# Performance work log

Hardware: AMD Instinct MI355X
Metric: run time of the kernel (lower is better)

The kernel has to match this reference:

```python
import jax, jax.numpy as jnp
import numpy as np

N1, F_IN, E1 = 50000, 128, 1000000   # data1: 10 graphs x 5000 nodes
B, NPG = 10, 5000
N2, E2 = 199, 4000                    # data2: fixed by fc1 in-dim 9950 = 50*199
K = 50
LN_EPS = 1e-5


def setup_inputs() -> dict:
    key = jax.random.key(0)
    ks = jax.random.split(key, 24)
    s = lambda k, shape: (jax.random.normal(k, shape, jnp.float32) * 0.05)
    inp = {}
    inp["x1"] = jax.random.normal(ks[0], (N1, F_IN), jnp.float32)
    inp["edge_index1"] = jax.random.randint(ks[1], (2, E1), 0, N1, jnp.int32)
    inp["batch1"] = jnp.repeat(jnp.arange(B, dtype=jnp.int32), NPG)  # equal-size graphs
    inp["x2"] = jax.random.normal(ks[2], (N2, F_IN), jnp.float32)
    inp["edge_index2"] = jax.random.randint(ks[3], (2, E2), 0, N2, jnp.int32)
    # GNN params (shared Siamese weights). PyG SAGEConv: lin_l (aggr, has bias), lin_r (root, no bias)
    inp["w1l"] = s(ks[4], (128, F_IN)); inp["b1l"] = jnp.zeros((128,), jnp.float32)
    inp["w1r"] = s(ks[5], (128, F_IN))
    inp["w2l"] = s(ks[6], (64, 128));   inp["b2l"] = jnp.zeros((64,), jnp.float32)
    inp["w2r"] = s(ks[7], (64, 128))
    # MLP head
    inp["fc1_w"] = s(ks[8], (128, K * N2)); inp["fc1_b"] = jnp.zeros((128,), jnp.float32)
    inp["ln1_g"] = jnp.ones((128,), jnp.float32); inp["ln1_b"] = jnp.zeros((128,), jnp.float32)
    inp["fc2_w"] = s(ks[9], (64, 128)); inp["fc2_b"] = jnp.zeros((64,), jnp.float32)
    inp["ln2_g"] = jnp.ones((64,), jnp.float32); inp["ln2_b"] = jnp.zeros((64,), jnp.float32)
    inp["fc3_w"] = s(ks[10], (1, 64)); inp["fc3_b"] = jnp.zeros((1,), jnp.float32)
    return inp


def _sage(x, edge_index, wl, bl, wr, n_nodes):
    # mean aggregation of source features at target nodes, then two linears
    src, dst = edge_index[0], edge_index[1]
    msg_sum = jax.ops.segment_sum(x[src], dst, num_segments=n_nodes)
    cnt = jax.ops.segment_sum(jnp.ones((edge_index.shape[1], 1), x.dtype), dst,
                              num_segments=n_nodes)
    mean = msg_sum / jnp.maximum(cnt, 1.0)
    return mean @ wl.T + bl + x @ wr.T


def _gnn(x, ei, w1l, b1l, w1r, w2l, b2l, w2r):
    n = x.shape[0]
    h = jax.nn.relu(_sage(x, ei, w1l, b1l, w1r, n))
    return jax.nn.relu(_sage(h, ei, w2l, b2l, w2r, n))


def _layernorm(x, g, b):
    mu = jnp.mean(x, -1, keepdims=True)
    var = jnp.mean((x - mu) ** 2, -1, keepdims=True)
    return (x - mu) * jax.lax.rsqrt(var + LN_EPS) * g + b


def reference(x1, edge_index1, batch1, x2, edge_index2,
              w1l, b1l, w1r, w2l, b2l, w2r,
              fc1_w, fc1_b, ln1_g, ln1_b, fc2_w, fc2_b, ln2_g, ln2_b, fc3_w, fc3_b):
    out1 = _gnn(x1, edge_index1, w1l, b1l, w1r, w2l, b2l, w2r)   # [N1, 64]
    out2 = _gnn(x2, edge_index2, w1l, b1l, w1r, w2l, b2l, w2r)   # [N2, 64]
    # cdist p=2
    a2 = jnp.sum(out1 * out1, -1, keepdims=True)                 # [N1,1]
    b2 = jnp.sum(out2 * out2, -1)                                # [N2]
    d2 = a2 + b2[None, :] - 2.0 * (out1 @ out2.T)
    dist = jnp.sqrt(jnp.maximum(d2, 0.0))                        # [N1, N2]
    # SortAggregation(k=50): per-graph sort rows by last column (desc), take top k.
    # batch1 groups equal-size graphs contiguously -> reshape is exact dense batching.
    xb = dist.reshape(B, NPG, N2)
    order = jnp.argsort(-xb[:, :, -1], axis=1)[:, :K]            # [B, K]
    topk = jnp.take_along_axis(xb, order[:, :, None], axis=1)    # [B, K, N2]
    out = topk.reshape(B, K * N2)
    out = jax.nn.relu(_layernorm(out @ fc1_w.T + fc1_b, ln1_g, ln1_b))
    out = jax.nn.relu(_layernorm(out @ fc2_w.T + fc2_b, ln2_g, ln2_b))
    out = jax.nn.sigmoid(out @ fc3_w.T + fc3_b)                  # [B, 1]
    return out
```

## Files before the change

### kernel.cpp

```cpp
#include <hip/hip_runtime.h>
#include <math.h>

#define N1 50000
#define F_IN 128
#define E1 1000000
#define Bg 10
#define NPG 5000
#define N2 199
#define E2 4000
#define KSEL 50
#define LN_EPS 1e-5f
#define CHUNKS 16
#define CHSZ 313
#define EBT 4096
#define NB 196
#define BCAP 6144

typedef unsigned long long ull;

__global__ void k_bucket(const int* __restrict__ ei1, int* __restrict__ bcnt,
                         unsigned int* __restrict__ bed,
                         const int* __restrict__ ei2, int* __restrict__ rp2,
                         int* __restrict__ srcs2) {
  int t = threadIdx.x;
  int blk = blockIdx.x;
  const int nEdgeBlocks = (E1 + EBT - 1) / EBT;
  if (blk == nEdgeBlocks) {
    __shared__ int cnt2[N2];
    __shared__ int cur2[N2];
    const int* src = ei2;
    const int* dst = ei2 + E2;
    for (int i = t; i < N2; i += 256) cnt2[i] = 0;
    __syncthreads();
    for (int e = t; e < E2; e += 256) atomicAdd(&cnt2[dst[e]], 1);
    __syncthreads();
    if (t == 0) {
      int run = 0;
      rp2[0] = 0;
      for (int i = 0; i < N2; i++) {
        cur2[i] = run;
        run += cnt2[i];
        rp2[i + 1] = run;
      }
    }
    __syncthreads();
    for (int e = t; e < E2; e += 256) {
      int d = dst[e];
      int pos = atomicAdd(&cur2[d], 1);
      srcs2[pos] = src[e];
    }
    return;
  }
  __shared__ int hcnt[NB];
  const int* src = ei1;
  const int* dst = ei1 + E1;
  int e0 = blk * EBT;
  int e1 = min(e0 + EBT, E1);
  if (t < NB) hcnt[t] = 0;
  __syncthreads();
  for (int e = e0 + t; e < e1; e += 256) atomicAdd(&hcnt[dst[e] >> 8], 1);
  __syncthreads();
  if (t < NB) hcnt[t] = atomicAdd(&bcnt[t], hcnt[t]);
  __syncthreads();
  for (int e = e0 + t; e < e1; e += 256) {
    int d = dst[e];
    int s = src[e];
    int b = d >> 8;
    int pos = atomicAdd(&hcnt[b], 1);
    if (pos < BCAP)
      bed[(size_t)b * BCAP + pos] = ((unsigned int)(d & 255) << 16) | (unsigned int)s;
  }
}

__global__ __launch_bounds__(1024) void k_csr_bucket(
    const int* __restrict__ bcnt, const unsigned int* __restrict__ bed,
    int* __restrict__ rp, int* __restrict__ srcs) {
  __shared__ int cnt[256];
  __shared__ int cur[256];
  __shared__ int wsums[4];
  __shared__ int s_bbase;
  int b = blockIdx.x, t = threadIdx.x;
  int lane = t & 63, w = t >> 6;
  int total = min(bcnt[b], BCAP);
  if (t < 256) cnt[t] = 0;
  if (w == 0) {
    int vb = 0;
    for (int i = lane; i < b; i += 64) vb += min(bcnt[i], BCAP);
    for (int off = 32; off; off >>= 1) vb += __shfl_xor(vb, off);
    if (lane == 0) s_bbase = vb;
  }
  __syncthreads();
  const unsigned int* list = bed + (size_t)b * BCAP;
  for (int e = t; e < total; e += 1024) atomicAdd(&cnt[list[e] >> 16], 1);
  __syncthreads();
  int incl = 0, v = 0;
  if (t < 256) {
    v = cnt[t];
    int x = v;
#pragma unroll
    for (int off = 1; off < 64; off <<= 1) {
      int y = __shfl_up(x, off);
      if (lane >= off) x += y;
    }
    if (lane == 63) wsums[w] = x;
    incl = x;
  }
  __syncthreads();
  if (t < 256) {
    int pre = 0;
    for (int i = 0; i < w; i++) pre += wsums[i];
    incl += pre;
    int bbase = s_bbase;
    int node = b * 256 + t;
    if (node < N1) rp[node + 1] = bbase + incl;
    cur[t] = bbase + incl - v;
    if (b == 0 && t == 0) rp[0] = 0;
  }
  __syncthreads();
  for (int e = t; e < total; e += 1024) {
    unsigned int pe = list[e];
    int pos = atomicAdd(&cur[pe >> 16], 1);
    srcs[pos] = (int)(pe & 0xFFFFu);
  }
}

__global__ void k_aggr128(const float* __restrict__ xA, const int* __restrict__ rpA,
                          const int* __restrict__ srcsA, float* __restrict__ meanA, int nA,
                          const float* __restrict__ xB, const int* __restrict__ rpB,
                          const int* __restrict__ srcsB, float* __restrict__ meanB, int nB,
                          int blocksA) {
  int blk = blockIdx.x;
  const float* x;
  const int* rp;
  const int* srcs;
  float* mean;
  int n, nb0;
  if (blk < blocksA) { x = xA; rp = rpA; srcs = srcsA; mean = meanA; n = nA; nb0 = blk * 4; }
  else { x = xB; rp = rpB; srcs = srcsB; mean = meanB; n = nB; nb0 = (blk - blocksA) * 4; }
  int lane = threadIdx.x & 63;
  int node = nb0 + (threadIdx.x >> 6);
  if (node >= n) return;
  int s = rp[node], e = rp[node + 1];
  int deg = e - s;
  int half = lane >> 5;
  int sub = lane & 31;
  const float4* xp = (const float4*)x;
  float4 acc = make_float4(0.f, 0.f, 0.f, 0.f);
  int sv = 0;
  if (s + lane < e) sv = srcs[s + lane];
  int lim = deg < 64 ? deg : 64;
  int i = 0;
  for (; i + 8 <= lim; i += 8) {
    int s0 = __shfl(sv, i + half);
    int s1 = __shfl(sv, i + 2 + half);
    int s2 = __shfl(sv, i + 4 + half);
    int s3 = __shfl(sv, i + 6 + half);
    float4 v0 = xp[(size_t)s0 * 32 + sub];
    float4 v1 = xp[(size_t)s1 * 32 + sub];
    float4 v2 = xp[(size_t)s2 * 32 + sub];
    float4 v3 = xp[(size_t)s3 * 32 + sub];
    acc.x += (v0.x + v1.x) + (v2.x + v3.x);
    acc.y += (v0.y + v1.y) + (v2.y + v3.y);
    acc.z += (v0.z + v1.z) + (v2.z + v3.z);
    acc.w += (v0.w + v1.w) + (v2.w + v3.w);
  }
  for (; i + 2 <= lim; i += 2) {
    int s0 = __shfl(sv, i + half);
    float4 v = xp[(size_t)s0 * 32 + sub];
    acc.x += v.x; acc.y += v.y; acc.z += v.z; acc.w += v.w;
  }
  if (i < lim) {
    int s0 = __shfl(sv, i);
    if (half == 0) {
      float4 v = xp[(size_t)s0 * 32 + sub];
      acc.x += v.x; acc.y += v.y; acc.z += v.z; acc.w += v.w;
    }
    i = lim;
  }
  if (deg > 64) {
    int ii = s + 64;
    for (; ii + 8 <= e; ii += 8) {
      int s0 = srcs[ii + half];
      int s1 = srcs[ii + 2 + half];
      int s2 = srcs[ii + 4 + half];
      int s3 = srcs[ii + 6 + half];
      float4 v0 = xp[(size_t)s0 * 32 + sub];
      float4 v1 = xp[(size_t)s1 * 32 + sub];
      float4 v2 = xp[(size_t)s2 * 32 + sub];
      float4 v3 = xp[(size_t)s3 * 32 + sub];
      acc.x += (v0.x + v1.x) + (v2.x + v3.x);
      acc.y += (v0.y + v1.y) + (v2.y + v3.y);
      acc.z += (v0.z + v1.z) + (v2.z + v3.z);
      acc.w += (v0.w + v1.w) + (v2.w + v3.w);
    }
    for (; ii + 2 <= e; ii += 2) {
      int s0 = srcs[ii + half];
      float4 v = xp[(size_t)s0 * 32 + sub];
      acc.x += v.x; acc.y += v.y; acc.z += v.z; acc.w += v.w;
    }
    if (ii < e && half == 0) {
      float4 v = xp[(size_t)srcs[ii] * 32 + sub];
      acc.x += v.x; acc.y += v.y; acc.z += v.z; acc.w += v.w;
    }
  }
  acc.x += __shfl_xor(acc.x, 32);
  acc.y += __shfl_xor(acc.y, 32);
  acc.z += __shfl_xor(acc.z, 32);
  acc.w += __shfl_xor(acc.w, 32);
  if (half == 0) {
    float c = (float)(deg > 0 ? deg : 1);
    float inv = 1.f / c;
    float4 o = make_float4(acc.x * inv, acc.y * inv, acc.z * inv, acc.w * inv);
    ((float4*)mean)[(size_t)node * 32 + sub] = o;
  }
}

__global__ void k_aggr_fused64(const float* __restrict__ zA, const int* __restrict__ rpA,
                               const int* __restrict__ srcsA, float* __restrict__ outA, int nA,
                               const float* __restrict__ zB, const int* __restrict__ rpB,
                               const int* __restrict__ srcsB, float* __restrict__ outB, int nB,
                               const float* __restrict__ bias, int blocksA) {
  int blk = blockIdx.x;
  const float* zlr;
  const int* rp;
  const int* srcs;
  float* out;
  int n, nb0;
  if (blk < blocksA) { zlr = zA; rp = rpA; srcs = srcsA; out = outA; n = nA; nb0 = blk * 4; }
  else { zlr = zB; rp = rpB; srcs = srcsB; out = outB; n = nB; nb0 = (blk - blocksA) * 4; }
  int lane = threadIdx.x & 63;
  int node = nb0 + (threadIdx.x >> 6);
  if (node >= n) return;
  int s = rp[node], e = rp[node + 1];
  int deg = e - s;
  int q = lane >> 4;
  int sub = lane & 15;
  const float4* zp = (const float4*)zlr;
  float4 acc = make_float4(0.f, 0.f, 0.f, 0.f);
  int sv = 0;
  if (s + lane < e) sv = srcs[s + lane];
  int lim = deg < 64 ? deg : 64;
  int i = 0;
  for (; i + 8 <= lim; i += 8) {
    int s0 = __shfl(sv, i + q);
    int s1 = __shfl(sv, i + 4 + q);
    float4 v0 = zp[(size_t)s0 * 32 + sub];
    float4 v1 = zp[(size_t)s1 * 32 + sub];
    acc.x += v0.x + v1.x;
    acc.y += v0.y + v1.y;
    acc.z += v0.z + v1.z;
    acc.w += v0.w + v1.w;
  }
  for (; i + 4 <= lim; i += 4) {
    int s0 = __shfl(sv, i + q);
    float4 v = zp[(size_t)s0 * 32 + sub];
    acc.x += v.x; acc.y += v.y; acc.z += v.z; acc.w += v.w;
  }
  {
    int rem = lim - i;
    int s0 = __shfl(sv, i + q);
    if (q < rem) {
      float4 v = zp[(size_t)s0 * 32 + sub];
      acc.x += v.x; acc.y += v.y; acc.z += v.z; acc.w += v.w;
    }
    i = lim;
  }
  if (deg > 64) {
    int ii = s + 64;
    for (; ii + 8 <= e; ii += 8) {
      int s0 = srcs[ii + q];
      int s1 = srcs[ii + 4 + q];
      float4 v0 = zp[(size_t)s0 * 32 + sub];
      float4 v1 = zp[(size_t)s1 * 32 + sub];
      acc.x += v0.x + v1.x;
      acc.y += v0.y + v1.y;
      acc.z += v0.z + v1.z;
      acc.w += v0.w + v1.w;
    }
    for (; ii + 4 <= e; ii += 4) {
      int s0 = srcs[ii + q];
      float4 v = zp[(size_t)s0 * 32 + sub];
      acc.x += v.x; acc.y += v.y; acc.z += v.z; acc.w += v.w;
    }
    int rem = e - ii;
    if (q < rem) {
      int s0 = srcs[ii + q];
      float4 v = zp[(size_t)s0 * 32 + sub];
      acc.x += v.x; acc.y += v.y; acc.z += v.z; acc.w += v.w;
    }
  }
  acc.x += __shfl_xor(acc.x, 16);
  acc.y += __shfl_xor(acc.y, 16);
  acc.z += __shfl_xor(acc.z, 16);
  acc.w += __shfl_xor(acc.w, 16);
  acc.x += __shfl_xor(acc.x, 32);
  acc.y += __shfl_xor(acc.y, 32);
  acc.z += __shfl_xor(acc.z, 32);
  acc.w += __shfl_xor(acc.w, 32);
  if (q == 0) {
    float c = (float)(deg > 0 ? deg : 1);
    float inv = 1.f / c;
    float4 mb = ((const float4*)bias)[sub];
    float4 rt = zp[(size_t)node * 32 + 16 + sub];
    float v0 = acc.x * inv + mb.x + rt.x;
    float v1 = acc.y * inv + mb.y + rt.y;
    float v2 = acc.z * inv + mb.z + rt.z;
    float v3 = acc.w * inv + mb.w + rt.w;
    float4 o;
    o.x = v0 > 0.f ? v0 : 0.f;
    o.y = v1 > 0.f ? v1 : 0.f;
    o.z = v2 > 0.f ? v2 : 0.f;
    o.w = v3 > 0.f ? v3 : 0.f;
    ((float4*)out)[(size_t)node * 16 + sub] = o;
  }
}

__global__ __launch_bounds__(256) void k_sage_lin(
    const float* __restrict__ xinA, const float* __restrict__ meanA,
    float* __restrict__ zA, int nA,
    const float* __restrict__ xinB, const float* __restrict__ meanB,
    float* __restrict__ zB, int nB,
    const float* __restrict__ w1l, const float* __restrict__ b1l,
    const float* __restrict__ w1r,
    const float* __restrict__ w2l, const float* __restrict__ w2r, int blocksA) {
  constexpr int TM = 128, TK = 32;
  constexpr int SA = TM + 4;
  constexpr int SW = 128 + 4;
  __shared__ float s_a[TK][SA];
  __shared__ float s_w[TK][SW];
  int blk = blockIdx.x;
  const float* xin;
  const float* mean;
  float* zlr;
  int n, m0;
  if (blk < blocksA) { xin = xinA; mean = meanA; zlr = zA; n = nA; m0 = blk * TM; }
  else { xin = xinB; mean = meanB; zlr = zB; n = nB; m0 = (blk - blocksA) * TM; }
  int t = threadIdx.x;
  int tx = t & 15, ty = t >> 4;
  int sub = t >> 3;
  int kv = (t & 7) << 2;

  float acc[8][8];
#pragma unroll
  for (int i = 0; i < 8; i++)
#pragma unroll
    for (int j = 0; j < 8; j++) acc[i][j] = 0.f;

  for (int ph = 0; ph < 2; ph++) {
    const float* A = ph ? xin : mean;
    const float* W = ph ? w1r : w1l;
    for (int k0 = 0; k0 < 128; k0 += TK) {
      __syncthreads();
#pragma unroll
      for (int p = 0; p < 4; p++) {
        int node = m0 + p * 32 + sub;
        float4 v = make_float4(0.f, 0.f, 0.f, 0.f);
        if (node < n) v = *(const float4*)&A[(size_t)node * 128 + k0 + kv];
        int col = p * 32 + sub;
        s_a[kv + 0][col] = v.x;
        s_a[kv + 1][col] = v.y;
        s_a[kv + 2][col] = v.z;
        s_a[kv + 3][col] = v.w;
      }
#pragma unroll
      for (int p = 0; p < 4; p++) {
        int j = p * 32 + sub;
        float4 v = *(const float4*)&W[(size_t)j * 128 + k0 + kv];
        s_w[kv + 0][j] = v.x;
        s_w[kv + 1][j] = v.y;
        s_w[kv + 2][j] = v.z;
        s_w[kv + 3][j] = v.w;
      }
      __syncthreads();
#pragma unroll 8
      for (int kk = 0; kk < TK; kk++) {
        float4 a0 = *(const float4*)&s_a[kk][ty * 8];
        float4 a1 = *(const float4*)&s_a[kk][ty * 8 + 4];
        float av[8] = {a0.x, a0.y, a0.z, a0.w, a1.x, a1.y, a1.z, a1.w};
        float4 w0 = *(const float4*)&s_w[kk][tx * 8];
        float4 w1 = *(const float4*)&s_w[kk][tx * 8 + 4];
        float wv[8] = {w0.x, w0.y, w0.z, w0.w, w1.x, w1.y, w1.z, w1.w};
#pragma unroll
        for (int i = 0; i < 8; i++)
#pragma unroll
          for (int j = 0; j < 8; j++) acc[i][j] = fmaf(av[i], wv[j], acc[i][j]);
      }
    }
  }
  float h[8][8];
  {
    float bj[8];
#pragma unroll
    for (int j = 0; j < 8; j++) bj[j] = b1l[tx * 8 + j];
#pragma unroll
    for (int i = 0; i < 8; i++)
#pragma unroll
      for (int j = 0; j < 8; j++) {
        float v = acc[i][j] + bj[j];
        h[i][j] = v > 0.f ? v : 0.f;
        acc[i][j] = 0.f;
      }
  }
  for (int k0 = 0; k0 < 128; k0 += TK) {
    __syncthreads();
    int txk = tx - (k0 >> 3);
    if (txk >= 0 && txk < 4) {
#pragma unroll
      for (int i = 0; i < 8; i++)
#pragma unroll
        for (int j = 0; j < 8; j++) s_a[txk * 8 + j][ty * 8 + i] = h[i][j];
    }
#pragma unroll
    for (int p = 0; p < 4; p++) {
      int j = p * 32 + sub;
      const float* W = (j < 64) ? &w2l[(size_t)j * 128] : &w2r[(size_t)(j - 64) * 128];
      float4 v = *(const float4*)&W[k0 + kv];
      s_w[kv + 0][j] = v.x;
      s_w[kv + 1][j] = v.y;
      s_w[kv + 2][j] = v.z;
      s_w[kv + 3][j] = v.w;
    }
    __syncthreads();
#pragma unroll 8
    for (int kk = 0; kk < TK; kk++) {
      float4 a0 = *(const float4*)&s_a[kk][ty * 8];
      float4 a1 = *(const float4*)&s_a[kk][ty * 8 + 4];
      float av[8] = {a0.x, a0.y, a0.z, a0.w, a1.x, a1.y, a1.z, a1.w};
      float4 w0 = *(const float4*)&s_w[kk][tx * 8];
      float4 w1 = *(const float4*)&s_w[kk][tx * 8 + 4];
      float wv[8] = {w0.x, w0.y, w0.z, w0.w, w1.x, w1.y, w1.z, w1.w};
#pragma unroll
      for (int i = 0; i < 8; i++)
#pragma unroll
        for (int j = 0; j < 8; j++) acc[i][j] = fmaf(av[i], wv[j], acc[i][j]);
    }
  }
#pragma unroll
  for (int i = 0; i < 8; i++) {
    int node = m0 + ty * 8 + i;
    if (node < n) {
#pragma unroll
      for (int q = 0; q < 8; q += 4) {
        float4 o = make_float4(acc[i][q + 0], acc[i][q + 1], acc[i][q + 2], acc[i][q + 3]);
        *(float4*)&zlr[(size_t)node * 128 + tx * 8 + q] = o;
      }
    }
  }
}

__global__ void k_score_topk_local(const float* __restrict__ out1,
                                   const float* __restrict__ out2,
                                   ull* __restrict__ cand) {
  __shared__ ull s[512];
  __shared__ float brow[64];
  int blk = blockIdx.x;
  int b = blk >> 4, c = blk & 15;
  int t = threadIdx.x;
  if (t < 64) brow[t] = out2[198 * 64 + t];
  __syncthreads();
  const float4* b4 = (const float4*)brow;
  float b2 = 0.f;
#pragma unroll
  for (int q = 0; q < 16; q++) {
    float4 w = b4[q];
    b2 = fmaf(w.x, w.x, fmaf(w.y, w.y, fmaf(w.z, w.z, fmaf(w.w, w.w, b2))));
  }
#pragma unroll
  for (int p = 0; p < 2; p++) {
    int i = p * 256 + t;
    ull key = 0ULL;
    int gidx = c * CHSZ + i;
    if (i < CHSZ && gidx < NPG) {
      const float4* ap = (const float4*)&out1[((size_t)b * NPG + gidx) * 64];
      float dot = 0.f, a2 = 0.f;
#pragma unroll
      for (int q = 0; q < 16; q++) {
        float4 a = ap[q];
        float4 w = b4[q];
        dot = fmaf(a.x, w.x, fmaf(a.y, w.y, fmaf(a.z, w.z, fmaf(a.w, w.w, dot))));
        a2 = fmaf(a.x, a.x, fmaf(a.y, a.y, fmaf(a.z, a.z, fmaf(a.w, a.w, a2))));
      }
      float d2 = a2 + b2 - 2.f * dot;
      float sc = sqrtf(fmaxf(d2, 0.f));
      key = ((ull)__float_as_uint(sc) << 32) | (unsigned int)(~gidx);
    }
    s[i] = key;
  }
  __syncthreads();
  for (int k = 2; k <= 512; k <<= 1) {
    for (int j = k >> 1; j > 0; j >>= 1) {
#pragma unroll
      for (int p = 0; p < 2; p++) {
        int i = p * 256 + t;
        int l = i ^ j;
        if (l > i) {
          bool up = ((i & k) != 0);
          ull a = s[i], bb = s[l];
          if ((a > bb) == up) { s[i] = bb; s[l] = a; }
        }
      }
      __syncthreads();
    }
  }
  if (t < KSEL) cand[(b * CHUNKS + c) * KSEL + t] = s[t];
}

__global__ void k_topk_merge(const ull* __restrict__ cand, int* __restrict__ sel) {
  __shared__ ull s[1024];
  int b = blockIdx.x, t = threadIdx.x;
#pragma unroll
  for (int p = 0; p < 4; p++) {
    int i = p * 256 + t;
    s[i] = (i < CHUNKS * KSEL) ? cand[b * CHUNKS * KSEL + i] : 0ULL;
  }
  __syncthreads();
  for (int k = 2; k <= 1024; k <<= 1) {
    for (int j = k >> 1; j > 0; j >>= 1) {
#pragma unroll
      for (int p = 0; p < 4; p++) {
        int i = p * 256 + t;
        int l = i ^ j;
        if (l > i) {
          bool up = ((i & k) != 0);
          ull a = s[i], bb = s[l];
          if ((a > bb) == up) { s[i] = bb; s[l] = a; }
        }
      }
      __syncthreads();
    }
  }
  if (t < KSEL) {
    int gidx = (int)(~((unsigned int)s[t]));
    sel[b * KSEL + t] = b * NPG + gidx;
  }
}

__global__ void k_dist_rows(const float* __restrict__ out1, const float* __restrict__ out2,
                            const int* __restrict__ sel, float* __restrict__ D) {
  __shared__ float arow[64];
  int i = blockIdx.x;
  int t = threadIdx.x;
  int node = sel[i];
  if (t < 64) arow[t] = out1[(size_t)node * 64 + t];
  __syncthreads();
  float a2 = 0.f;
#pragma unroll
  for (int f = 0; f < 64; f++) a2 = fmaf(arow[f], arow[f], a2);
  for (int nn = t; nn < N2; nn += 256) {
    float dot = 0.f, b2 = 0.f;
#pragma unroll 8
    for (int f = 0; f < 64; f++) {
      float bv = out2[nn * 64 + f];
      dot = fmaf(arow[f], bv, dot);
      b2 = fmaf(bv, bv, b2);
    }
    float d2 = a2 + b2 - 2.f * dot;
    D[i * N2 + nn] = sqrtf(fmaxf(d2, 0.f));
  }
}

__global__ void k_fc1_dot(const float* __restrict__ D, const float* __restrict__ w,
                          float* __restrict__ h1pre) {
  constexpr int M = KSEL * N2;
  constexpr int M2 = M / 2;
  int j = blockIdx.x;
  int t = threadIdx.x;
  const float2* wp = (const float2*)(w + (size_t)j * M);
  float acc[Bg];
#pragma unroll
  for (int b = 0; b < Bg; b++) acc[b] = 0.f;
  for (int m = t; m < M2; m += 256) {
    float2 wv = wp[m];
#pragma unroll
    for (int b = 0; b < Bg; b++) {
      float2 dv = ((const float2*)(D + (size_t)b * M))[m];
      acc[b] = fmaf(dv.x, wv.x, fmaf(dv.y, wv.y, acc[b]));
    }
  }
  __shared__ float ws_[4][Bg];
  int lane = t & 63, wv_ = t >> 6;
#pragma unroll
  for (int b = 0; b < Bg; b++) {
    float v = acc[b];
    for (int off = 32; off; off >>= 1) v += __shfl_xor(v, off);
    if (lane == 0) ws_[wv_][b] = v;
  }
  __syncthreads();
  if (t < Bg) h1pre[t * 128 + j] = ws_[0][t] + ws_[1][t] + ws_[2][t] + ws_[3][t];
}

__global__ void k_fc123(const float* __restrict__ h1pre, const float* __restrict__ fc1b,
                        const float* __restrict__ g1, const float* __restrict__ be1,
                        const float* __restrict__ w2, const float* __restrict__ b2v,
                        const float* __restrict__ g2, const float* __restrict__ be2,
                        const float* __restrict__ w3, const float* __restrict__ b3,
                        float* __restrict__ out) {
  __shared__ float wsum[2];
  __shared__ float sh[128];
  int b = blockIdx.x, t = threadIdx.x;
  float acc = h1pre[b * 128 + t] + fc1b[t];
  int lane = t & 63, wv_ = t >> 6;
  float ssum = acc;
  for (int off = 32; off; off >>= 1) ssum += __shfl_xor(ssum, off);
  if (lane == 0) wsum[wv_] = ssum;
  __syncthreads();
  float mu = (wsum[0] + wsum[1]) / 128.f;
  __syncthreads();
  float d = acc - mu;
  float vv = d * d;
  for (int off = 32; off; off >>= 1) vv += __shfl_xor(vv, off);
  if (lane == 0) wsum[wv_] = vv;
  __syncthreads();
  float var = (wsum[0] + wsum[1]) / 128.f;
  float r = rsqrtf(var + LN_EPS);
  float h = d * r * g1[t] + be1[t];
  sh[t] = h > 0.f ? h : 0.f;
  __syncthreads();
  if (t < 64) {
    float a2 = b2v[t];
#pragma unroll 8
    for (int k = 0; k < 128; k++) a2 = fmaf(sh[k], w2[t * 128 + k], a2);
    float s2 = a2;
    for (int off = 32; off; off >>= 1) s2 += __shfl_xor(s2, off);
    float mu2 = s2 * (1.f / 64.f);
    float d2 = a2 - mu2;
    float vv2 = d2 * d2;
    for (int off = 32; off; off >>= 1) vv2 += __shfl_xor(vv2, off);
    float r2 = rsqrtf(vv2 * (1.f / 64.f) + LN_EPS);
    float h2 = d2 * r2 * g2[t] + be2[t];
    h2 = h2 > 0.f ? h2 : 0.f;
    float pp = h2 * w3[t];
    for (int off = 32; off; off >>= 1) pp += __shfl_xor(pp, off);
    if (t == 0) out[b] = 1.f / (1.f + expf(-(pp + b3[0])));
  }
}

extern "C" void kernel_launch(void* const* d_in, const int* in_sizes, int n_in,
                              void* d_out, int out_size, void* d_ws, size_t ws_size,
                              hipStream_t stream) {
  const float* x1 = (const float*)d_in[0];
  const int* ei1 = (const int*)d_in[1];
  const float* x2 = (const float*)d_in[3];
  const int* ei2 = (const int*)d_in[4];
  const float* w1l = (const float*)d_in[5];
  const float* b1l = (const float*)d_in[6];
  const float* w1r = (const float*)d_in[7];
  const float* w2l = (const float*)d_in[8];
  const float* b2l = (const float*)d_in[9];
  const float* w2r = (const float*)d_in[10];
  const float* fc1w = (const float*)d_in[11];
  const float* fc1b = (const float*)d_in[12];
  const float* ln1g = (const float*)d_in[13];
  const float* ln1b = (const float*)d_in[14];
  const float* fc2w = (const float*)d_in[15];
  const float* fc2b = (const float*)d_in[16];
  const float* ln2g = (const float*)d_in[17];
  const float* ln2b = (const float*)d_in[18];
  const float* fc3w = (const float*)d_in[19];
  const float* fc3b = (const float*)d_in[20];
  float* out = (float*)d_out;

  char* p = (char*)d_ws;
  auto alloc = [&](size_t bytes) {
    char* r = p;
    p += (bytes + 255) & ~(size_t)255;
    return r;
  };
  int* rp1 = (int*)alloc((N1 + 1) * 4);
  int* bcnt = (int*)alloc(NB * 4);
  unsigned int* bed = (unsigned int*)alloc((size_t)NB * BCAP * 4);
  int* srcs1 = (int*)alloc((size_t)E1 * 4);
  int* rp2 = (int*)alloc((N2 + 1) * 4);
  int* srcs2 = (int*)alloc(E2 * 4);
  float* bufMean = (float*)alloc((size_t)N1 * 128 * 4);
  float* bufZ = (float*)alloc((size_t)N1 * 128 * 4);
  float* out1b = (float*)alloc((size_t)N1 * 64 * 4);
  float* mean2 = (float*)alloc((size_t)N2 * 128 * 4);
  float* z2g = (float*)alloc((size_t)N2 * 128 * 4);
  float* out2b = (float*)alloc((size_t)N2 * 64 * 4);
  int* sel = (int*)alloc(Bg * KSEL * 4);
  ull* cand = (ull*)alloc((size_t)Bg * CHUNKS * KSEL * 8);
  float* Dm = (float*)alloc((size_t)Bg * KSEL * N2 * 4);
  float* h1pre = (float*)alloc(Bg * 128 * 4);

  const int nEdgeBlocks = (E1 + EBT - 1) / EBT;
  const int aggrBlocksA = (N1 + 3) / 4;
  const int aggrBlocksB = (N2 + 3) / 4;
  const int gemmBlocksA = (N1 + 127) / 128;
  const int gemmBlocksB = (N2 + 127) / 128;

  hipMemsetAsync(bcnt, 0, NB * 4, stream);
  k_bucket<<<nEdgeBlocks + 1, 256, 0, stream>>>(ei1, bcnt, bed, ei2, rp2, srcs2);
  k_csr_bucket<<<NB, 1024, 0, stream>>>(bcnt, bed, rp1, srcs1);
  k_aggr128<<<aggrBlocksA + aggrBlocksB, 256, 0, stream>>>(
      x1, rp1, srcs1, bufMean, N1, x2, rp2, srcs2, mean2, N2, aggrBlocksA);
  k_sage_lin<<<gemmBlocksA + gemmBlocksB, 256, 0, stream>>>(
      x1, bufMean, bufZ, N1, x2, mean2, z2g, N2, w1l, b1l, w1r, w2l, w2r, gemmBlocksA);
  k_aggr_fused64<<<aggrBlocksA + aggrBlocksB, 256, 0, stream>>>(
      bufZ, rp1, srcs1, out1b, N1, z2g, rp2, srcs2, out2b, N2, b2l, aggrBlocksA);
  k_score_topk_local<<<Bg * CHUNKS, 256, 0, stream>>>(out1b, out2b, cand);
  k_topk_merge<<<Bg, 256, 0, stream>>>(cand, sel);
  k_dist_rows<<<Bg * KSEL, 256, 0, stream>>>(out1b, out2b, sel, Dm);
  k_fc1_dot<<<128, 256, 0, stream>>>(Dm, fc1w, h1pre);
  k_fc123<<<Bg, 128, 0, stream>>>(h1pre, fc1b, ln1g, ln1b, fc2w, fc2b, ln2g, ln2b,
                                  fc3w, fc3b, out);
}
```

Measured before the change: 386.1 us.

## Register-prefetch next K-chunk in fused SAGE linear and pad weight smem layout

Merges the three GEMM phases of the fused SAGE linear kernel into one 12-chunk loop that loads the next chunk's activation and weight tiles into registers while the current chunk is computed. This aims to hide global-memory latency behind the FMA loop. It also remaps the shared weight tile to a 12-float stride per thread group to reduce LDS bank conflicts on the float4 reads. The register prefetch buffers plus h and acc raise register pressure, which may lower occupancy.

```diff
diff --git a/kernel.cpp b/kernel.cpp
--- a/kernel.cpp
+++ b/kernel.cpp
@@ -325,9 +325,9 @@
     const float* __restrict__ w2l, const float* __restrict__ w2r, int blocksA) {
   constexpr int TM = 128, TK = 32;
   constexpr int SA = TM + 4;
-  constexpr int SW = 128 + 4;
+  constexpr int SWS = 196;
   __shared__ float s_a[TK][SA];
-  __shared__ float s_w[TK][SW];
+  __shared__ float s_w[TK][SWS];
   int blk = blockIdx.x;
   const float* xin;
   const float* mean;
@@ -339,86 +339,73 @@
   int tx = t & 15, ty = t >> 4;
   int sub = t >> 3;
   int kv = (t & 7) << 2;
+  int wg = sub >> 3, wo = sub & 7;
 
   float acc[8][8];
 #pragma unroll
   for (int i = 0; i < 8; i++)
 #pragma unroll
     for (int j = 0; j < 8; j++) acc[i][j] = 0.f;
-
-  for (int ph = 0; ph < 2; ph++) {
-    const float* A = ph ? xin : mean;
-    const float* W = ph ? w1r : w1l;
-    for (int k0 = 0; k0 < 128; k0 += TK) {
-      __syncthreads();
+  float h[8][8];
+  float4 ra[4], rw[4];
+
+#pragma unroll
+  for (int p = 0; p < 4; p++) {
+    int node = m0 + p * 32 + sub;
+    ra[p] = make_float4(0.f, 0.f, 0.f, 0.f);
+    if (node < n) ra[p] = *(const float4*)&mean[(size_t)node * 128 + kv];
+    rw[p] = *(const float4*)&w1l[(size_t)(p * 32 + sub) * 128 + kv];
+  }
+
+  for (int c = 0; c < 12; c++) {
+    __syncthreads();
+    if (c < 8) {
 #pragma unroll
       for (int p = 0; p < 4; p++) {
-        int node = m0 + p * 32 + sub;
-        float4 v = make_float4(0.f, 0.f, 0.f, 0.f);
-        if (node < n) v = *(const float4*)&A[(size_t)node * 128 + k0 + kv];
         int col = p * 32 + sub;
-        s_a[kv + 0][col] = v.x;
-        s_a[kv + 1][col] = v.y;
-        s_a[kv + 2][col] = v.z;
-        s_a[kv + 3][col] = v.w;
+        s_a[kv + 0][col] = ra[p].x;
+        s_a[kv + 1][col] = ra[p].y;
+        s_a[kv + 2][col] = ra[p].z;
+        s_a[kv + 3][col] = ra[p].w;
       }
-#pragma unroll
-      for (int p = 0; p < 4; p++) {
-        int j = p * 32 + sub;
-        float4 v = *(const float4*)&W[(size_t)j * 128 + k0 + kv];
-        s_w[kv + 0][j] = v.x;
-        s_w[kv + 1][j] = v.y;
-        s_w[kv + 2][j] = v.z;
-        s_w[kv + 3][j] = v.w;
+    } else {
+      int txk = tx - (c - 8) * 4;
+      if (txk >= 0 && txk < 4) {
+#pragma unroll
+        for (int i = 0; i < 8; i++)
+#pragma unroll
+          for (int j = 0; j < 8; j++) s_a[txk * 8 + j][ty * 8 + i] = h[i][j];
       }
-      __syncthreads();
-#pragma unroll 8
-      for (int kk = 0; kk < TK; kk++) {
-        float4 a0 = *(const float4*)&s_a[kk][ty * 8];
-        float4 a1 = *(const float4*)&s_a[kk][ty * 8 + 4];
-        float av[8] = {a0.x, a0.y, a0.z, a0.w, a1.x, a1.y, a1.z, a1.w};
-        float4 w0 = *(const float4*)&s_w[kk][tx * 8];
-        float4 w1 = *(const float4*)&s_w[kk][tx * 8 + 4];
-        float wv[8] = {w0.x, w0.y, w0.z, w0.w, w1.x, w1.y, w1.z, w1.w};
-#pragma unroll
-        for (int i = 0; i < 8; i++)
-#pragma unroll
-          for (int j = 0; j < 8; j++) acc[i][j] = fmaf(av[i], wv[j], acc[i][j]);
+    }
+#pragma unroll
+    for (int p = 0; p < 4; p++) {
+      int col = (p * 4 + wg) * 12 + wo;
+      s_w[kv + 0][col] = rw[p].x;
+      s_w[kv + 1][col] = rw[p].y;
+      s_w[kv + 2][col] = rw[p].z;
+      s_w[kv + 3][col] = rw[p].w;
+    }
+    int cn = c + 1;
+    if (cn < 12) {
+      int k0n = (cn & 3) * 32;
+      if (cn < 8) {
+        const float* A = (cn < 4) ? mean : xin;
+        const float* W = (cn < 4) ? w1l : w1r;
+#pragma unroll
+        for (int p = 0; p < 4; p++) {
+          int node = m0 + p * 32 + sub;
+          ra[p] = make_float4(0.f, 0.f, 0.f, 0.f);
+          if (node < n) ra[p] = *(const float4*)&A[(size_t)node * 128 + k0n + kv];
+          rw[p] = *(const float4*)&W[(size_t)(p * 32 + sub) * 128 + k0n + kv];
+        }
+      } else {
+#pragma unroll
+        for (int p = 0; p < 4; p++) {
+          int j = p * 32 + sub;
+          const float* W = (j < 64) ? &w2l[(size_t)j * 128] : &w2r[(size_t)(j - 64) * 128];
+          rw[p] = *(const float4*)&W[k0n + kv];
+        }
       }
-    }
-  }
-  float h[8][8];
-  {
-    float bj[8];
-#pragma unroll
-    for (int j = 0; j < 8; j++) bj[j] = b1l[tx * 8 + j];
-#pragma unroll
-    for (int i = 0; i < 8; i++)
-#pragma unroll
-      for (int j = 0; j < 8; j++) {
-        float v = acc[i][j] + bj[j];
-        h[i][j] = v > 0.f ? v : 0.f;
-        acc[i][j] = 0.f;
-      }
-  }
-  for (int k0 = 0; k0 < 128; k0 += TK) {
-    __syncthreads();
-    int txk = tx - (k0 >> 3);
-    if (txk >= 0 && txk < 4) {
-#pragma unroll
-      for (int i = 0; i < 8; i++)
-#pragma unroll
-        for (int j = 0; j < 8; j++) s_a[txk * 8 + j][ty * 8 + i] = h[i][j];
-    }
-#pragma unroll
-    for (int p = 0; p < 4; p++) {
-      int j = p * 32 + sub;
-      const float* W = (j < 64) ? &w2l[(size_t)j * 128] : &w2r[(size_t)(j - 64) * 128];
-      float4 v = *(const float4*)&W[k0 + kv];
-      s_w[kv + 0][j] = v.x;
-      s_w[kv + 1][j] = v.y;
-      s_w[kv + 2][j] = v.z;
-      s_w[kv + 3][j] = v.w;
     }
     __syncthreads();
 #pragma unroll 8
@@ -426,13 +413,26 @@
       float4 a0 = *(const float4*)&s_a[kk][ty * 8];
       float4 a1 = *(const float4*)&s_a[kk][ty * 8 + 4];
       float av[8] = {a0.x, a0.y, a0.z, a0.w, a1.x, a1.y, a1.z, a1.w};
-      float4 w0 = *(const float4*)&s_w[kk][tx * 8];
-      float4 w1 = *(const float4*)&s_w[kk][tx * 8 + 4];
+      float4 w0 = *(const float4*)&s_w[kk][tx * 12];
+      float4 w1 = *(const float4*)&s_w[kk][tx * 12 + 4];
       float wv[8] = {w0.x, w0.y, w0.z, w0.w, w1.x, w1.y, w1.z, w1.w};
 #pragma unroll
       for (int i = 0; i < 8; i++)
 #pragma unroll
         for (int j = 0; j < 8; j++) acc[i][j] = fmaf(av[i], wv[j], acc[i][j]);
+    }
+    if (c == 7) {
+      float bj[8];
+#pragma unroll
+      for (int j = 0; j < 8; j++) bj[j] = b1l[tx * 8 + j];
+#pragma unroll
+      for (int i = 0; i < 8; i++)
+#pragma unroll
+        for (int j = 0; j < 8; j++) {
+          float v = acc[i][j] + bj[j];
+          h[i][j] = v > 0.f ? v : 0.f;
+          acc[i][j] = 0.f;
+        }
     }
   }
 #pragma unroll
```

Result: no change. 387.4 us (median of 2 runs) (+0.3%).
